# Kernel tuning notes

Hardware: AMD Instinct MI355X
Metric: run time of the kernel (lower is better)

The kernel has to match this reference:

```python
import jax, jax.numpy as jnp
import numpy as np

LN_EPS = 1e-5
SLOPE = 0.01  # LeakyReLU default

def _ln(x, g, b):
    m = x.mean(-1, keepdims=True)
    v = ((x - m) ** 2).mean(-1, keepdims=True)
    return (x - m) / jnp.sqrt(v + LN_EPS) * g + b

def _leaky(x):
    return jnp.where(x >= 0, x, SLOPE * x)

def _lstm(x_seq, h0, c0, Wih, Whh, bih, bhh):
    # x_seq: [B,S,E]; PyTorch gate order i,f,g,o. Returns (hT, per-step hiddens [B,S,H]).
    gx = jnp.einsum('bse,ge->bsg', x_seq, Wih) + bih + bhh  # precompute input projections
    def step(carry, gxt):
        h, c = carry
        gates = gxt + h @ Whh.T
        i, f, g, o = jnp.split(gates, 4, axis=-1)
        c = jax.nn.sigmoid(f) * c + jax.nn.sigmoid(i) * jnp.tanh(g)
        h = jax.nn.sigmoid(o) * jnp.tanh(c)
        return (h, c), h
    (hT, _), hs = jax.lax.scan(step, (h0, c0), gx.transpose(1, 0, 2))
    return hT, hs.transpose(1, 0, 2)

def setup_inputs() -> dict:
    B, S, NF, E, H, L, C = 256, 1024, 32, 64, 128, 64, 31
    key = jax.random.key(0)
    ks = iter(jax.random.split(key, 40))
    rn = lambda shape, s=0.08: (jax.random.normal(next(ks), shape, jnp.float32) * s)
    d = {}
    d['x'] = jax.random.normal(next(ks), (B, S, NF), jnp.float32)
    d['eps'] = jax.random.normal(next(ks), (B, L), jnp.float32)
    d['init_W'] = rn((E, NF)); d['init_b'] = rn((E,)); d['init_g'] = jnp.ones((E,)); d['init_beta'] = jnp.zeros((E,))
    d['enc_Wih'] = rn((4 * H, E)); d['enc_Whh'] = rn((4 * H, H)); d['enc_bih'] = rn((4 * H,)); d['enc_bhh'] = rn((4 * H,))
    d['mu_W'] = rn((L, H)); d['mu_b'] = rn((L,)); d['mu_g'] = jnp.ones((L,)); d['mu_beta'] = jnp.zeros((L,))
    d['lv_W'] = rn((L, H)); d['lv_b'] = rn((L,)); d['lv_g'] = jnp.ones((L,)); d['lv_beta'] = jnp.zeros((L,))
    d['dec_Wih'] = rn((4 * H, E)); d['dec_Whh'] = rn((4 * H, H)); d['dec_bih'] = rn((4 * H,)); d['dec_bhh'] = rn((4 * H,))
    d['lh_W'] = rn((H, L)); d['lh_b'] = rn((H,)); d['lh_g'] = jnp.ones((H,)); d['lh_beta'] = jnp.zeros((H,))
    d['lc_W'] = rn((H, L)); d['lc_b'] = rn((H,)); d['lc_g'] = jnp.ones((H,)); d['lc_beta'] = jnp.zeros((H,))
    d['act_W'] = rn((C, H)); d['act_b'] = rn((C,))
    d['time_W'] = rn((1, H)); d['time_b'] = rn((1,))
    return d

def reference(x, eps, init_W, init_b, init_g, init_beta,
              enc_Wih, enc_Whh, enc_bih, enc_bhh,
              mu_W, mu_b, mu_g, mu_beta, lv_W, lv_b, lv_g, lv_beta,
              dec_Wih, dec_Whh, dec_bih, dec_bhh,
              lh_W, lh_b, lh_g, lh_beta, lc_W, lc_b, lc_g, lc_beta,
              act_W, act_b, time_W, time_b):
    B = x.shape[0]
    H = enc_Whh.shape[1]
    # init_layers: Linear -> LeakyReLU -> LayerNorm
    x_emb = _ln(_leaky(x @ init_W.T + init_b), init_g, init_beta)  # [B,S,E]
    # encoder LSTM with h0=ones, c0=zeros (as in encode())
    hT, _ = _lstm(x_emb, jnp.ones((B, H), x.dtype), jnp.zeros((B, H), x.dtype),
                  enc_Wih, enc_Whh, enc_bih, enc_bhh)
    mu = _ln(_leaky(hT @ mu_W.T + mu_b), mu_g, mu_beta)
    logvar = _ln(_leaky(hT @ lv_W.T + lv_b), lv_g, lv_beta)
    latent = mu + eps * jnp.exp(0.5 * logvar)
    # decoder init state from latent
    dh0 = _ln(_leaky(latent @ lh_W.T + lh_b), lh_g, lh_beta)
    dc0 = _ln(_leaky(latent @ lc_W.T + lc_b), lc_g, lc_beta)
    # _decode prefix loop (prefix_len=1..S-1, collecting hn) == one scan over x_emb[:, :S-1]
    _, hs = _lstm(x_emb[:, :-1], dh0, dc0, dec_Wih, dec_Whh, dec_bih, dec_bhh)  # [B,S-1,H]
    acts = hs @ act_W.T + act_b   # [B,S-1,C]
    ts = hs @ time_W.T + time_b   # [B,S-1,1]
    return acts, ts, mu, logvar
```

## Files before the change

kernel.cpp:

```cpp
#include <hip/hip_runtime.h>
#include <hip/hip_bf16.h>
#include <type_traits>


#define B_ 256
#define S_ 1024
#define NF_ 32
#define E_ 64
#define H_ 128
#define L_ 64
#define C_ 31

#define ACTS_OFF 0
#define TS_OFF   8118528
#define MU_OFF   8380416
#define LV_OFF   8396800

#define LOG2E  1.44269504f
#define LOG2E2 2.88539008f

typedef __attribute__((ext_vector_type(8))) short short8;
typedef __attribute__((ext_vector_type(4))) float float4v;

__device__ inline unsigned short f2bf(float x){
  union { float f; unsigned u; } a; a.f = x;
  unsigned r = a.u + 0x7FFFu + ((a.u >> 16) & 1u);
  return (unsigned short)(r >> 16);
}
__device__ inline float frcp(float x){
#if __has_builtin(__builtin_amdgcn_rcpf)
  return __builtin_amdgcn_rcpf(x);
#else
  return 1.0f / x;
#endif
}
__device__ inline float fexp2(float x){
#if __has_builtin(__builtin_amdgcn_exp2f)
  return __builtin_amdgcn_exp2f(x);
#else
  return exp2f(x);
#endif
}
__device__ inline float fsig(float x){ return frcp(1.0f + fexp2(-LOG2E*x)); }
__device__ inline float leaky(float x){ return x >= 0.0f ? x : 0.01f*x; }
__device__ inline float wredsum(float v){
  v += __shfl_xor(v, 32, 64);
  v += __shfl_xor(v, 16, 64);
  v += __shfl_xor(v,  8, 64);
  v += __shfl_xor(v,  4, 64);
  v += __shfl_xor(v,  2, 64);
  v += __shfl_xor(v,  1, 64);
  return v;
}

#define INIT_ROWS 16
__global__ __launch_bounds__(256) void init_kernel(
    const float* __restrict__ x, const float* __restrict__ W,
    const float* __restrict__ bias, const float* __restrict__ gam,
    const float* __restrict__ beta, unsigned short* __restrict__ xemb)
{
  if (blockIdx.x == 0 && threadIdx.x < 64)
    xemb[(size_t)S_*B_*E_ + threadIdx.x] = 0;

  const int wave = threadIdx.x >> 6, lane = threadIdx.x & 63;
  float wf[NF_];
  {
    const float4* wr = (const float4*)(W + lane * NF_);
    #pragma unroll
    for (int j = 0; j < NF_/4; ++j){
      float4 t = wr[j];
      wf[4*j+0] = t.x; wf[4*j+1] = t.y; wf[4*j+2] = t.z; wf[4*j+3] = t.w;
    }
  }
  const float bb = bias[lane], gg = gam[lane], be = beta[lane];

  const int r0 = (blockIdx.x * 4 + wave) * INIT_ROWS;
  for (int rr = 0; rr < INIT_ROWS; ++rr){
    const int ru = __builtin_amdgcn_readfirstlane(r0 + rr);
    const int b = ru >> 10, s = ru & 1023;
    const float* xr = x + (size_t)ru * NF_;
    float acc = bb;
    #pragma unroll
    for (int k = 0; k < NF_; ++k)
      acc = fmaf(xr[k], wf[k], acc);
    acc = leaky(acc);
    float m = wredsum(acc) * (1.0f/64.0f);
    float d = acc - m;
    float v = wredsum(d*d) * (1.0f/64.0f);
    float y = d * rsqrtf(v + 1e-5f) * gg + be;
    xemb[((size_t)s * B_ + b) * E_ + lane] = f2bf(y);
  }
}

__global__ __launch_bounds__(512, 2) void lstm_kernel(
    const float* __restrict__ Wih,
    const float* __restrict__ Whh,
    const float* __restrict__ bih, const float* __restrict__ bhh,
    const unsigned short* __restrict__ xemb,
    int T,
    const float* __restrict__ h0, const float* __restrict__ c0,
    float* __restrict__ hT_out,
    float* __restrict__ outp,
    const float* __restrict__ actW, const float* __restrict__ actB,
    const float* __restrict__ timeW, const float* __restrict__ timeB)
{
  __shared__ unsigned short hbuf[2][16*136];
  const int tid = threadIdx.x;
  const int wave = tid >> 6, lane = tid & 63;
  const int q = lane >> 4, c16 = lane & 15;
  const int bt0 = blockIdx.x * 4;
  const int hu = wave * 16 + c16;

  short8 Bf[4][6];
  float bias[4];
  #pragma unroll
  for (int g = 0; g < 4; ++g){
    const int gcol = g*128 + hu;
    bias[g] = bih[gcol] + bhh[gcol];
    #pragma unroll
    for (int kb = 0; kb < 6; ++kb){
      union { short8 v; unsigned short u[8]; } tmp;
      #pragma unroll
      for (int j = 0; j < 8; ++j){
        int k = kb*32 + q*8 + j;
        float wv = (kb < 4) ? Whh[gcol*H_ + k] : Wih[gcol*E_ + (k - H_)];
        tmp.u[j] = f2bf(wv);
      }
      Bf[g][kb] = tmp.v;
    }
  }

  const bool do_out = (outp != nullptr) && (wave < 2);
  short8 Of0 = 0, Of1 = 0, Of2 = 0, Of3 = 0;
  float obias = 0.0f;
  if (do_out){
    const int n = wave*16 + c16;
    obias = (n < C_) ? actB[n] : timeB[0];
    union { short8 v; unsigned short u[8]; } tmp[4];
    #pragma unroll
    for (int kb = 0; kb < 4; ++kb)
      #pragma unroll
      for (int j = 0; j < 8; ++j){
        int k = kb*32 + q*8 + j;
        tmp[kb].u[j] = f2bf((n < C_) ? actW[n*H_ + k] : timeW[k]);
      }
    Of0 = tmp[0].v; Of1 = tmp[1].v; Of2 = tmp[2].v; Of3 = tmp[3].v;
  }

  unsigned short* hflat = &hbuf[0][0];
  for (int idx = tid; idx < 2*16*136; idx += 512) hflat[idx] = 0;
  __syncthreads();
  {
    int b = tid >> 7, k = tid & 127;
    hbuf[0][(4*b)*136 + k] = h0 ? f2bf(h0[((size_t)(bt0 + b))*H_ + k])
                                : (unsigned short)0x3F80;
  }
  float cst = c0 ? c0[((size_t)(bt0 + q))*H_ + hu] : 0.0f;
  __syncthreads();

  const int xb = c16 >> 2, xdt = c16 & 3;
  const unsigned short* xbase = xemb + ((size_t)(bt0 + xb))*E_ + q*8;
  const size_t xrow = (size_t)B_*E_;
  auto xwin = [&](int wt)->const unsigned short*{
    int tt = wt + xdt; if (tt > T-1) tt = T-1;
    return xbase + (size_t)tt * xrow;
  };

  float4v gxA[4], gxB[4];
  short8 nx0, nx1;
  { const unsigned short* p = xwin(0);
    nx0 = *(const short8*)p; nx1 = *(const short8*)(p + 32); }
  #pragma unroll
  for (int g = 0; g < 4; ++g){
    float4v t = (float4v){bias[g], bias[g], bias[g], bias[g]};
    t = __builtin_amdgcn_mfma_f32_16x16x32_bf16(nx0, Bf[g][4], t, 0, 0, 0);
    gxA[g] = __builtin_amdgcn_mfma_f32_16x16x32_bf16(nx1, Bf[g][5], t, 0, 0, 0);
  }
  { const unsigned short* p = xwin(4);
    nx0 = *(const short8*)p; nx1 = *(const short8*)(p + 32); }

  short8 Af0 = 0, Af1 = 0, Af2 = 0, Af3 = 0;
  short8 Po0 = 0, Po1 = 0, Po2 = 0, Po3 = 0;

  const unsigned short* haR0 = hflat + (c16 & ~3)*136 + q*8;
  const unsigned short* haR1 = haR0 + 2176;
  unsigned short* hw0 = hflat + (4*q)*136 + hu;
  unsigned short* hw1 = hw0 + 2176;
  float zero_f = 0.0f;
  const float4v z4 = (float4v){0.0f, 0.0f, 0.0f, 0.0f};

  auto out_head = [&](const unsigned short* ha, int tt_){
    if ((c16 & 3) == 0){
      Po0 = *(const short8*)(ha);
      Po1 = *(const short8*)(ha + 32);
      Po2 = *(const short8*)(ha + 64);
      Po3 = *(const short8*)(ha + 96);
    }
    float4v o = z4;
    o = __builtin_amdgcn_mfma_f32_16x16x32_bf16(Po0, Of0, o, 0, 0, 0);
    o = __builtin_amdgcn_mfma_f32_16x16x32_bf16(Po1, Of1, o, 0, 0, 0);
    o = __builtin_amdgcn_mfma_f32_16x16x32_bf16(Po2, Of2, o, 0, 0, 0);
    o = __builtin_amdgcn_mfma_f32_16x16x32_bf16(Po3, Of3, o, 0, 0, 0);
    const float val = o[0] + obias;
    const int n = wave*16 + c16;
    const size_t bq = (size_t)(bt0 + q);
    if (n < C_) outp[ACTS_OFF + (bq*(S_-1) + (size_t)tt_)*C_ + n] = val;
    else        outp[TS_OFF + bq*(S_-1) + (size_t)tt_] = val;
  };

  auto step = [&](int t, auto dtc, float4v (&gxP)[4], auto&& pre, auto&& post){
    constexpr int dt = decltype(dtc)::value;
    const unsigned short* ha = (t & 1) ? haR1 : haR0;
    if ((c16 & 3) == dt){
      Af0 = *(const short8*)(ha);
      Af1 = *(const short8*)(ha + 32);
      Af2 = *(const short8*)(ha + 64);
      Af3 = *(const short8*)(ha + 96);
    }
    pre();
    if (do_out && t > 0) out_head(ha, t - 1);

    float4v aA[4], aB[4];
    #pragma unroll
    for (int g = 0; g < 4; ++g)
      aA[g] = __builtin_amdgcn_mfma_f32_16x16x32_bf16(Af0, Bf[g][0], gxP[g], 0, 0, 0);
    #pragma unroll
    for (int g = 0; g < 4; ++g)
      aB[g] = __builtin_amdgcn_mfma_f32_16x16x32_bf16(Af2, Bf[g][2], z4, 0, 0, 0);
    #pragma unroll
    for (int g = 0; g < 4; ++g)
      aA[g] = __builtin_amdgcn_mfma_f32_16x16x32_bf16(Af1, Bf[g][1], aA[g], 0, 0, 0);
    #pragma unroll
    for (int g = 0; g < 4; ++g)
      aB[g] = __builtin_amdgcn_mfma_f32_16x16x32_bf16(Af3, Bf[g][3], aB[g], 0, 0, 0);

    post();

    float gi = aA[0][dt] + aB[0][dt];
    float gf = aA[1][dt] + aB[1][dt];
    float gg = aA[2][dt] + aB[2][dt];
    float go = aA[3][dt] + aB[3][dt];
    float ei  = fexp2(gi * LOG2E);
    float e2g = fexp2(gg * LOG2E2);
    float t1  = (ei * (e2g - 1.0f)) * frcp((1.0f + ei) * (1.0f + e2g));
    float sf  = fsig(gf);
    float c   = fmaf(sf, cst, t1);
    cst = c;
    float eo  = fexp2(go * LOG2E);
    float e2c = fexp2(fminf(c * LOG2E2, 126.0f));
    float h   = (eo * (e2c - 1.0f)) * frcp((1.0f + eo) * (1.0f + e2c));
    unsigned vv;
    asm("v_cvt_pk_bf16_f32 %0, %1, %2" : "=v"(vv) : "v"(h), "v"(zero_f));
    unsigned short hb16 = (unsigned short)vv;
    unsigned short* hw = (t & 1) ? hw0 : hw1;
    hw[0] = hb16;
    if (hT_out && t == T-1) hT_out[((size_t)(bt0 + q))*H_ + hu] = h;
    __builtin_amdgcn_sched_barrier(0);
    asm volatile("s_waitcnt lgkmcnt(0)" ::: "memory");
    __builtin_amdgcn_s_barrier();
    __builtin_amdgcn_sched_barrier(0);
  };

  using I0 = std::integral_constant<int,0>;
  using I1 = std::integral_constant<int,1>;
  using I2 = std::integral_constant<int,2>;
  using I3 = std::integral_constant<int,3>;
  auto nop = []{};

  const int nwin = T >> 2, ntail = T & 3;
  for (int w = 0; w < nwin; ++w){
    const int t0 = w << 2;
    step(t0+0, I0{}, gxA, [&]{
      #pragma unroll
      for (int g = 0; g < 4; ++g){
        float4v tt = (float4v){bias[g], bias[g], bias[g], bias[g]};
        tt = __builtin_amdgcn_mfma_f32_16x16x32_bf16(nx0, Bf[g][4], tt, 0, 0, 0);
        gxB[g] = __builtin_amdgcn_mfma_f32_16x16x32_bf16(nx1, Bf[g][5], tt, 0, 0, 0);
      }
    }, nop);
    step(t0+1, I1{}, gxA, [&]{
      const unsigned short* p = xwin(t0 + 8);
      nx0 = *(const short8*)p; nx1 = *(const short8*)(p + 32);
    }, nop);
    step(t0+2, I2{}, gxA, nop, nop);
    step(t0+3, I3{}, gxA, nop, [&]{
      #pragma unroll
      for (int g = 0; g < 4; ++g) gxA[g] = gxB[g];
    });
  }
  if (ntail > 0) step(nwin*4+0, I0{}, gxA, nop, nop);
  if (ntail > 1) step(nwin*4+1, I1{}, gxA, nop, nop);
  if (ntail > 2) step(nwin*4+2, I2{}, gxA, nop, nop);

  if (do_out) out_head((T & 1) ? haR1 : haR0, T - 1);
}

__global__ __launch_bounds__(128) void latent_kernel(
    const float* __restrict__ hT, const float* __restrict__ eps,
    const float* __restrict__ mu_W, const float* __restrict__ mu_b,
    const float* __restrict__ mu_g, const float* __restrict__ mu_be,
    const float* __restrict__ lv_W, const float* __restrict__ lv_b,
    const float* __restrict__ lv_g, const float* __restrict__ lv_be,
    const float* __restrict__ lh_W, const float* __restrict__ lh_b,
    const float* __restrict__ lh_g, const float* __restrict__ lh_be,
    const float* __restrict__ lc_W, const float* __restrict__ lc_b,
    const float* __restrict__ lc_g, const float* __restrict__ lc_be,
    float* __restrict__ out, float* __restrict__ dh0, float* __restrict__ dc0)
{
  const int b = blockIdx.x, tid = threadIdx.x;
  const int wave = tid >> 6, lane = tid & 63;
  __shared__ float shT[H_];
  __shared__ float smu[L_], slv[L_], slat[L_];
  __shared__ float part[2];
  shT[tid] = hT[(size_t)b*H_ + tid];
  __syncthreads();
  {
    const float* W = wave ? lv_W : mu_W;
    float a = (wave ? lv_b : mu_b)[lane];
    for (int k = 0; k < H_; ++k) a += shT[k] * W[lane*H_ + k];
    a = leaky(a);
    float m = wredsum(a) * (1.0f/L_);
    float d = a - m;
    float v = wredsum(d*d) * (1.0f/L_);
    float y = d * rsqrtf(v + 1e-5f) * (wave ? lv_g : mu_g)[lane] + (wave ? lv_be : mu_be)[lane];
    out[(wave ? LV_OFF : MU_OFF) + (size_t)b*L_ + lane] = y;
    if (wave) slv[lane] = y; else smu[lane] = y;
  }
  __syncthreads();
  if (tid < L_) slat[tid] = smu[tid] + eps[(size_t)b*L_ + tid] * expf(0.5f*slv[tid]);
  __syncthreads();
  #pragma unroll 1
  for (int which = 0; which < 2; ++which){
    const float* W = which ? lc_W : lh_W;
    float p = (which ? lc_b : lh_b)[tid];
    for (int k = 0; k < L_; ++k) p += slat[k] * W[tid*L_ + k];
    p = leaky(p);
    float s = wredsum(p);
    if (lane == 0) part[wave] = s;
    __syncthreads();
    float mean = (part[0] + part[1]) * (1.0f/H_);
    __syncthreads();
    float d = p - mean;
    float s2 = wredsum(d*d);
    if (lane == 0) part[wave] = s2;
    __syncthreads();
    float var = (part[0] + part[1]) * (1.0f/H_);
    __syncthreads();
    float y = d * rsqrtf(var + 1e-5f) * (which ? lc_g : lh_g)[tid] + (which ? lc_be : lh_be)[tid];
    (which ? dc0 : dh0)[(size_t)b*H_ + tid] = y;
  }
}

extern "C" void kernel_launch(void* const* d_in, const int* in_sizes, int n_in,
                              void* d_out, int out_size, void* d_ws, size_t ws_size,
                              hipStream_t stream)
{
  (void)in_sizes; (void)n_in; (void)out_size; (void)ws_size;
  const float* x       = (const float*)d_in[0];
  const float* eps     = (const float*)d_in[1];
  const float* init_W  = (const float*)d_in[2];
  const float* init_b  = (const float*)d_in[3];
  const float* init_g  = (const float*)d_in[4];
  const float* init_be = (const float*)d_in[5];
  const float* enc_Wih = (const float*)d_in[6];
  const float* enc_Whh = (const float*)d_in[7];
  const float* enc_bih = (const float*)d_in[8];
  const float* enc_bhh = (const float*)d_in[9];
  const float* mu_W  = (const float*)d_in[10];
  const float* mu_b  = (const float*)d_in[11];
  const float* mu_g  = (const float*)d_in[12];
  const float* mu_be = (const float*)d_in[13];
  const float* lv_W  = (const float*)d_in[14];
  const float* lv_b  = (const float*)d_in[15];
  const float* lv_g  = (const float*)d_in[16];
  const float* lv_be = (const float*)d_in[17];
  const float* dec_Wih = (const float*)d_in[18];
  const float* dec_Whh = (const float*)d_in[19];
  const float* dec_bih = (const float*)d_in[20];
  const float* dec_bhh = (const float*)d_in[21];
  const float* lh_W  = (const float*)d_in[22];
  const float* lh_b  = (const float*)d_in[23];
  const float* lh_g  = (const float*)d_in[24];
  const float* lh_be = (const float*)d_in[25];
  const float* lc_W  = (const float*)d_in[26];
  const float* lc_b  = (const float*)d_in[27];
  const float* lc_g  = (const float*)d_in[28];
  const float* lc_be = (const float*)d_in[29];
  const float* act_W  = (const float*)d_in[30];
  const float* act_b  = (const float*)d_in[31];
  const float* time_W = (const float*)d_in[32];
  const float* time_b = (const float*)d_in[33];
  float* out = (float*)d_out;

  unsigned short* xemb = (unsigned short*)d_ws;
  float* hT  = (float*)(xemb + (size_t)S_*B_*E_ + 64);
  float* dh0 = hT  + B_*H_;
  float* dc0 = dh0 + B_*H_;

  init_kernel<<<dim3((B_*S_)/(4*INIT_ROWS)), dim3(256), 0, stream>>>(
      x, init_W, init_b, init_g, init_be, xemb);

  lstm_kernel<<<dim3(64), dim3(512), 0, stream>>>(
      enc_Wih, enc_Whh, enc_bih, enc_bhh, xemb, S_,
      nullptr, nullptr, hT,
      nullptr, nullptr, nullptr, nullptr, nullptr);

  latent_kernel<<<dim3(B_), dim3(128), 0, stream>>>(
      hT, eps, mu_W, mu_b, mu_g, mu_be, lv_W, lv_b, lv_g, lv_be,
      lh_W, lh_b, lh_g, lh_be, lc_W, lc_b, lc_g, lc_be, out, dh0, dc0);

  lstm_kernel<<<dim3(64), dim3(512), 0, stream>>>(
      dec_Wih, dec_Whh, dec_bih, dec_bhh, xemb, S_-1,
      dh0, dc0, nullptr,
      out, act_W, act_b, time_W, time_b);
}
```

Baseline: 1.220 ms.

## Fuse encoder, latent, and decoder into one persistent kernel with batched output head

Merges the encoder LSTM, latent/LayerNorm stage, and decoder LSTM into a single kernel. Intermediate state (hT, dh0, dc0) stays in shared memory, which removes two launches and the global round-trips between them. The per-step output head is replaced by a history buffer in shared memory, so one MFMA sequence produces four timesteps of acts/ts every four steps instead of one output per step. This adds shared-memory use and register pressure, and the latent stage now runs on only 64 blocks.

```diff
diff --git a/kernel.cpp b/kernel.cpp
--- a/kernel.cpp
+++ b/kernel.cpp
@@ -92,211 +92,13 @@
   }
 }
 
-__global__ __launch_bounds__(512, 2) void lstm_kernel(
-    const float* __restrict__ Wih,
-    const float* __restrict__ Whh,
-    const float* __restrict__ bih, const float* __restrict__ bhh,
+__global__ __launch_bounds__(512, 2) void mega_kernel(
     const unsigned short* __restrict__ xemb,
-    int T,
-    const float* __restrict__ h0, const float* __restrict__ c0,
-    float* __restrict__ hT_out,
-    float* __restrict__ outp,
-    const float* __restrict__ actW, const float* __restrict__ actB,
-    const float* __restrict__ timeW, const float* __restrict__ timeB)
-{
-  __shared__ unsigned short hbuf[2][16*136];
-  const int tid = threadIdx.x;
-  const int wave = tid >> 6, lane = tid & 63;
-  const int q = lane >> 4, c16 = lane & 15;
-  const int bt0 = blockIdx.x * 4;
-  const int hu = wave * 16 + c16;
-
-  short8 Bf[4][6];
-  float bias[4];
-  #pragma unroll
-  for (int g = 0; g < 4; ++g){
-    const int gcol = g*128 + hu;
-    bias[g] = bih[gcol] + bhh[gcol];
-    #pragma unroll
-    for (int kb = 0; kb < 6; ++kb){
-      union { short8 v; unsigned short u[8]; } tmp;
-      #pragma unroll
-      for (int j = 0; j < 8; ++j){
-        int k = kb*32 + q*8 + j;
-        float wv = (kb < 4) ? Whh[gcol*H_ + k] : Wih[gcol*E_ + (k - H_)];
-        tmp.u[j] = f2bf(wv);
-      }
-      Bf[g][kb] = tmp.v;
-    }
-  }
-
-  const bool do_out = (outp != nullptr) && (wave < 2);
-  short8 Of0 = 0, Of1 = 0, Of2 = 0, Of3 = 0;
-  float obias = 0.0f;
-  if (do_out){
-    const int n = wave*16 + c16;
-    obias = (n < C_) ? actB[n] : timeB[0];
-    union { short8 v; unsigned short u[8]; } tmp[4];
-    #pragma unroll
-    for (int kb = 0; kb < 4; ++kb)
-      #pragma unroll
-      for (int j = 0; j < 8; ++j){
-        int k = kb*32 + q*8 + j;
-        tmp[kb].u[j] = f2bf((n < C_) ? actW[n*H_ + k] : timeW[k]);
-      }
-    Of0 = tmp[0].v; Of1 = tmp[1].v; Of2 = tmp[2].v; Of3 = tmp[3].v;
-  }
-
-  unsigned short* hflat = &hbuf[0][0];
-  for (int idx = tid; idx < 2*16*136; idx += 512) hflat[idx] = 0;
-  __syncthreads();
-  {
-    int b = tid >> 7, k = tid & 127;
-    hbuf[0][(4*b)*136 + k] = h0 ? f2bf(h0[((size_t)(bt0 + b))*H_ + k])
-                                : (unsigned short)0x3F80;
-  }
-  float cst = c0 ? c0[((size_t)(bt0 + q))*H_ + hu] : 0.0f;
-  __syncthreads();
-
-  const int xb = c16 >> 2, xdt = c16 & 3;
-  const unsigned short* xbase = xemb + ((size_t)(bt0 + xb))*E_ + q*8;
-  const size_t xrow = (size_t)B_*E_;
-  auto xwin = [&](int wt)->const unsigned short*{
-    int tt = wt + xdt; if (tt > T-1) tt = T-1;
-    return xbase + (size_t)tt * xrow;
-  };
-
-  float4v gxA[4], gxB[4];
-  short8 nx0, nx1;
-  { const unsigned short* p = xwin(0);
-    nx0 = *(const short8*)p; nx1 = *(const short8*)(p + 32); }
-  #pragma unroll
-  for (int g = 0; g < 4; ++g){
-    float4v t = (float4v){bias[g], bias[g], bias[g], bias[g]};
-    t = __builtin_amdgcn_mfma_f32_16x16x32_bf16(nx0, Bf[g][4], t, 0, 0, 0);
-    gxA[g] = __builtin_amdgcn_mfma_f32_16x16x32_bf16(nx1, Bf[g][5], t, 0, 0, 0);
-  }
-  { const unsigned short* p = xwin(4);
-    nx0 = *(const short8*)p; nx1 = *(const short8*)(p + 32); }
-
-  short8 Af0 = 0, Af1 = 0, Af2 = 0, Af3 = 0;
-  short8 Po0 = 0, Po1 = 0, Po2 = 0, Po3 = 0;
-
-  const unsigned short* haR0 = hflat + (c16 & ~3)*136 + q*8;
-  const unsigned short* haR1 = haR0 + 2176;
-  unsigned short* hw0 = hflat + (4*q)*136 + hu;
-  unsigned short* hw1 = hw0 + 2176;
-  float zero_f = 0.0f;
-  const float4v z4 = (float4v){0.0f, 0.0f, 0.0f, 0.0f};
-
-  auto out_head = [&](const unsigned short* ha, int tt_){
-    if ((c16 & 3) == 0){
-      Po0 = *(const short8*)(ha);
-      Po1 = *(const short8*)(ha + 32);
-      Po2 = *(const short8*)(ha + 64);
-      Po3 = *(const short8*)(ha + 96);
-    }
-    float4v o = z4;
-    o = __builtin_amdgcn_mfma_f32_16x16x32_bf16(Po0, Of0, o, 0, 0, 0);
-    o = __builtin_amdgcn_mfma_f32_16x16x32_bf16(Po1, Of1, o, 0, 0, 0);
-    o = __builtin_amdgcn_mfma_f32_16x16x32_bf16(Po2, Of2, o, 0, 0, 0);
-    o = __builtin_amdgcn_mfma_f32_16x16x32_bf16(Po3, Of3, o, 0, 0, 0);
-    const float val = o[0] + obias;
-    const int n = wave*16 + c16;
-    const size_t bq = (size_t)(bt0 + q);
-    if (n < C_) outp[ACTS_OFF + (bq*(S_-1) + (size_t)tt_)*C_ + n] = val;
-    else        outp[TS_OFF + bq*(S_-1) + (size_t)tt_] = val;
-  };
-
-  auto step = [&](int t, auto dtc, float4v (&gxP)[4], auto&& pre, auto&& post){
-    constexpr int dt = decltype(dtc)::value;
-    const unsigned short* ha = (t & 1) ? haR1 : haR0;
-    if ((c16 & 3) == dt){
-      Af0 = *(const short8*)(ha);
-      Af1 = *(const short8*)(ha + 32);
-      Af2 = *(const short8*)(ha + 64);
-      Af3 = *(const short8*)(ha + 96);
-    }
-    pre();
-    if (do_out && t > 0) out_head(ha, t - 1);
-
-    float4v aA[4], aB[4];
-    #pragma unroll
-    for (int g = 0; g < 4; ++g)
-      aA[g] = __builtin_amdgcn_mfma_f32_16x16x32_bf16(Af0, Bf[g][0], gxP[g], 0, 0, 0);
-    #pragma unroll
-    for (int g = 0; g < 4; ++g)
-      aB[g] = __builtin_amdgcn_mfma_f32_16x16x32_bf16(Af2, Bf[g][2], z4, 0, 0, 0);
-    #pragma unroll
-    for (int g = 0; g < 4; ++g)
-      aA[g] = __builtin_amdgcn_mfma_f32_16x16x32_bf16(Af1, Bf[g][1], aA[g], 0, 0, 0);
-    #pragma unroll
-    for (int g = 0; g < 4; ++g)
-      aB[g] = __builtin_amdgcn_mfma_f32_16x16x32_bf16(Af3, Bf[g][3], aB[g], 0, 0, 0);
-
-    post();
-
-    float gi = aA[0][dt] + aB[0][dt];
-    float gf = aA[1][dt] + aB[1][dt];
-    float gg = aA[2][dt] + aB[2][dt];
-    float go = aA[3][dt] + aB[3][dt];
-    float ei  = fexp2(gi * LOG2E);
-    float e2g = fexp2(gg * LOG2E2);
-    float t1  = (ei * (e2g - 1.0f)) * frcp((1.0f + ei) * (1.0f + e2g));
-    float sf  = fsig(gf);
-    float c   = fmaf(sf, cst, t1);
-    cst = c;
-    float eo  = fexp2(go * LOG2E);
-    float e2c = fexp2(fminf(c * LOG2E2, 126.0f));
-    float h   = (eo * (e2c - 1.0f)) * frcp((1.0f + eo) * (1.0f + e2c));
-    unsigned vv;
-    asm("v_cvt_pk_bf16_f32 %0, %1, %2" : "=v"(vv) : "v"(h), "v"(zero_f));
-    unsigned short hb16 = (unsigned short)vv;
-    unsigned short* hw = (t & 1) ? hw0 : hw1;
-    hw[0] = hb16;
-    if (hT_out && t == T-1) hT_out[((size_t)(bt0 + q))*H_ + hu] = h;
-    __builtin_amdgcn_sched_barrier(0);
-    asm volatile("s_waitcnt lgkmcnt(0)" ::: "memory");
-    __builtin_amdgcn_s_barrier();
-    __builtin_amdgcn_sched_barrier(0);
-  };
-
-  using I0 = std::integral_constant<int,0>;
-  using I1 = std::integral_constant<int,1>;
-  using I2 = std::integral_constant<int,2>;
-  using I3 = std::integral_constant<int,3>;
-  auto nop = []{};
-
-  const int nwin = T >> 2, ntail = T & 3;
-  for (int w = 0; w < nwin; ++w){
-    const int t0 = w << 2;
-    step(t0+0, I0{}, gxA, [&]{
-      #pragma unroll
-      for (int g = 0; g < 4; ++g){
-        float4v tt = (float4v){bias[g], bias[g], bias[g], bias[g]};
-        tt = __builtin_amdgcn_mfma_f32_16x16x32_bf16(nx0, Bf[g][4], tt, 0, 0, 0);
-        gxB[g] = __builtin_amdgcn_mfma_f32_16x16x32_bf16(nx1, Bf[g][5], tt, 0, 0, 0);
-      }
-    }, nop);
-    step(t0+1, I1{}, gxA, [&]{
-      const unsigned short* p = xwin(t0 + 8);
-      nx0 = *(const short8*)p; nx1 = *(const short8*)(p + 32);
-    }, nop);
-    step(t0+2, I2{}, gxA, nop, nop);
-    step(t0+3, I3{}, gxA, nop, [&]{
-      #pragma unroll
-      for (int g = 0; g < 4; ++g) gxA[g] = gxB[g];
-    });
-  }
-  if (ntail > 0) step(nwin*4+0, I0{}, gxA, nop, nop);
-  if (ntail > 1) step(nwin*4+1, I1{}, gxA, nop, nop);
-  if (ntail > 2) step(nwin*4+2, I2{}, gxA, nop, nop);
-
-  if (do_out) out_head((T & 1) ? haR1 : haR0, T - 1);
-}
-
-__global__ __launch_bounds__(128) void latent_kernel(
-    const float* __restrict__ hT, const float* __restrict__ eps,
+    const float* __restrict__ encWih, const float* __restrict__ encWhh,
+    const float* __restrict__ encbih, const float* __restrict__ encbhh,
+    const float* __restrict__ decWih, const float* __restrict__ decWhh,
+    const float* __restrict__ decbih, const float* __restrict__ decbhh,
+    const float* __restrict__ eps,
     const float* __restrict__ mu_W, const float* __restrict__ mu_b,
     const float* __restrict__ mu_g, const float* __restrict__ mu_be,
     const float* __restrict__ lv_W, const float* __restrict__ lv_b,
@@ -305,50 +107,293 @@
     const float* __restrict__ lh_g, const float* __restrict__ lh_be,
     const float* __restrict__ lc_W, const float* __restrict__ lc_b,
     const float* __restrict__ lc_g, const float* __restrict__ lc_be,
-    float* __restrict__ out, float* __restrict__ dh0, float* __restrict__ dc0)
+    const float* __restrict__ actW, const float* __restrict__ actB,
+    const float* __restrict__ timeW, const float* __restrict__ timeB,
+    float* __restrict__ out)
 {
-  const int b = blockIdx.x, tid = threadIdx.x;
+  __shared__ unsigned short hbuf[2][16*136];
+  __shared__ unsigned short hist[2][16*136];
+  __shared__ float shT[4][H_];
+  __shared__ float sml[4][2*L_];
+  __shared__ float slat[4][L_];
+  __shared__ float sdh[4][H_], sdc[4][H_];
+  __shared__ float partA[8];
+
+  const int tid = threadIdx.x;
   const int wave = tid >> 6, lane = tid & 63;
-  __shared__ float shT[H_];
-  __shared__ float smu[L_], slv[L_], slat[L_];
-  __shared__ float part[2];
-  shT[tid] = hT[(size_t)b*H_ + tid];
+  const int q = lane >> 4, c16 = lane & 15;
+  const int bt0 = blockIdx.x * 4;
+  const int hu = wave * 16 + c16;
+  unsigned short* hflat = &hbuf[0][0];
+  unsigned short* histf = &hist[0][0];
+  const float4v z4 = (float4v){0.0f, 0.0f, 0.0f, 0.0f};
+  float zero_f = 0.0f;
+
+  for (int idx = tid; idx < 2*16*136; idx += 512) hflat[idx] = 0;
   __syncthreads();
+
+  const int xb = c16 >> 2, xdt = c16 & 3;
+  const unsigned short* xbase = xemb + ((size_t)(bt0 + xb))*E_ + q*8;
+  const size_t xrow = (size_t)B_*E_;
+
+  using I0 = std::integral_constant<int,0>;
+  using I1 = std::integral_constant<int,1>;
+  using I2 = std::integral_constant<int,2>;
+  using I3 = std::integral_constant<int,3>;
+  auto nop = []{};
+
+  auto run = [&](const float* Wih, const float* Whh, const float* bih,
+                 const float* bhh, int T, auto decc){
+    constexpr bool DEC = decltype(decc)::value;
+
+    short8 Bf[4][6];
+    float bias[4];
+    #pragma unroll
+    for (int g = 0; g < 4; ++g){
+      const int gcol = g*128 + hu;
+      bias[g] = bih[gcol] + bhh[gcol];
+      #pragma unroll
+      for (int kb = 0; kb < 6; ++kb){
+        union { short8 v; unsigned short u[8]; } tmp;
+        #pragma unroll
+        for (int j = 0; j < 8; ++j){
+          int k = kb*32 + q*8 + j;
+          float wv = (kb < 4) ? Whh[gcol*H_ + k] : Wih[gcol*E_ + (k - H_)];
+          tmp.u[j] = f2bf(wv);
+        }
+        Bf[g][kb] = tmp.v;
+      }
+    }
+
+    const bool do_head = DEC && (wave < 2);
+    short8 Of0 = 0, Of1 = 0, Of2 = 0, Of3 = 0;
+    float obias = 0.0f;
+    if (do_head){
+      const int n = wave*16 + c16;
+      obias = (n < C_) ? actB[n] : timeB[0];
+      union { short8 v; unsigned short u[8]; } tmp[4];
+      #pragma unroll
+      for (int kb = 0; kb < 4; ++kb)
+        #pragma unroll
+        for (int j = 0; j < 8; ++j){
+          int k = kb*32 + q*8 + j;
+          tmp[kb].u[j] = f2bf((n < C_) ? actW[n*H_ + k] : timeW[k]);
+        }
+      Of0 = tmp[0].v; Of1 = tmp[1].v; Of2 = tmp[2].v; Of3 = tmp[3].v;
+    }
+    short8 Ph0 = 0, Ph1 = 0, Ph2 = 0, Ph3 = 0;
+    float4v oacc = z4;
+
+    {
+      int b = tid >> 7, k = tid & 127;
+      hbuf[0][(4*b)*136 + k] = DEC ? f2bf(sdh[b][k]) : (unsigned short)0x3F80;
+    }
+    float cst = DEC ? sdc[q][hu] : 0.0f;
+    __syncthreads();
+
+    auto xwin = [&](int wt)->const unsigned short*{
+      int tt = wt + xdt; if (tt > T-1) tt = T-1;
+      return xbase + (size_t)tt * xrow;
+    };
+
+    float4v gxA[4], gxB[4];
+    short8 nx0, nx1;
+    { const unsigned short* p = xwin(0);
+      nx0 = *(const short8*)p; nx1 = *(const short8*)(p + 32); }
+    #pragma unroll
+    for (int g = 0; g < 4; ++g){
+      float4v t = (float4v){bias[g], bias[g], bias[g], bias[g]};
+      t = __builtin_amdgcn_mfma_f32_16x16x32_bf16(nx0, Bf[g][4], t, 0, 0, 0);
+      gxA[g] = __builtin_amdgcn_mfma_f32_16x16x32_bf16(nx1, Bf[g][5], t, 0, 0, 0);
+    }
+    { const unsigned short* p = xwin(4);
+      nx0 = *(const short8*)p; nx1 = *(const short8*)(p + 32); }
+
+    short8 Af0 = 0, Af1 = 0, Af2 = 0, Af3 = 0;
+
+    const unsigned short* haR0 = hflat + (c16 & ~3)*136 + q*8;
+    const unsigned short* haR1 = haR0 + 2176;
+    unsigned short* hw0 = hflat + (4*q)*136 + hu;
+    unsigned short* hw1 = hw0 + 2176;
+
+    auto step = [&](int t, auto dtc, float4v (&gxP)[4], auto&& pre, auto&& post){
+      constexpr int dt = decltype(dtc)::value;
+      const unsigned short* ha = (t & 1) ? haR1 : haR0;
+      if ((c16 & 3) == dt){
+        Af0 = *(const short8*)(ha);
+        Af1 = *(const short8*)(ha + 32);
+        Af2 = *(const short8*)(ha + 64);
+        Af3 = *(const short8*)(ha + 96);
+      }
+      pre();
+
+      float4v aA[4], aB[4];
+      #pragma unroll
+      for (int g = 0; g < 4; ++g)
+        aA[g] = __builtin_amdgcn_mfma_f32_16x16x32_bf16(Af0, Bf[g][0], gxP[g], 0, 0, 0);
+      #pragma unroll
+      for (int g = 0; g < 4; ++g)
+        aB[g] = __builtin_amdgcn_mfma_f32_16x16x32_bf16(Af2, Bf[g][2], z4, 0, 0, 0);
+      #pragma unroll
+      for (int g = 0; g < 4; ++g)
+        aA[g] = __builtin_amdgcn_mfma_f32_16x16x32_bf16(Af1, Bf[g][1], aA[g], 0, 0, 0);
+      #pragma unroll
+      for (int g = 0; g < 4; ++g)
+        aB[g] = __builtin_amdgcn_mfma_f32_16x16x32_bf16(Af3, Bf[g][3], aB[g], 0, 0, 0);
+
+      post();
+
+      float gi = aA[0][dt] + aB[0][dt];
+      float gf = aA[1][dt] + aB[1][dt];
+      float gg = aA[2][dt] + aB[2][dt];
+      float go = aA[3][dt] + aB[3][dt];
+      float ei  = fexp2(gi * LOG2E);
+      float e2g = fexp2(gg * LOG2E2);
+      float t1  = (ei * (e2g - 1.0f)) * frcp((1.0f + ei) * (1.0f + e2g));
+      float sf  = fsig(gf);
+      float c   = fmaf(sf, cst, t1);
+      cst = c;
+      float eo  = fexp2(go * LOG2E);
+      float e2c = fexp2(fminf(c * LOG2E2, 126.0f));
+      float h   = (eo * (e2c - 1.0f)) * frcp((1.0f + eo) * (1.0f + e2c));
+      unsigned vv;
+      asm("v_cvt_pk_bf16_f32 %0, %1, %2" : "=v"(vv) : "v"(h), "v"(zero_f));
+      unsigned short hb16 = (unsigned short)vv;
+      unsigned short* hw = (t & 1) ? hw0 : hw1;
+      hw[0] = hb16;
+      if (DEC)
+        histf[((t >> 2) & 1)*2176 + (4*q + dt)*136 + hu] = hb16;
+      if (!DEC && t == T-1) shT[q][hu] = h;
+      __builtin_amdgcn_sched_barrier(0);
+      asm volatile("s_waitcnt lgkmcnt(0)" ::: "memory");
+      __builtin_amdgcn_s_barrier();
+      __builtin_amdgcn_sched_barrier(0);
+    };
+
+    auto head_mfma = [&](int par){
+      const unsigned short* hb = histf + par*2176 + c16*136 + q*8;
+      Ph0 = *(const short8*)(hb);
+      Ph1 = *(const short8*)(hb + 32);
+      Ph2 = *(const short8*)(hb + 64);
+      Ph3 = *(const short8*)(hb + 96);
+      float4v o = (float4v){obias, obias, obias, obias};
+      o = __builtin_amdgcn_mfma_f32_16x16x32_bf16(Ph0, Of0, o, 0, 0, 0);
+      o = __builtin_amdgcn_mfma_f32_16x16x32_bf16(Ph1, Of1, o, 0, 0, 0);
+      o = __builtin_amdgcn_mfma_f32_16x16x32_bf16(Ph2, Of2, o, 0, 0, 0);
+      o = __builtin_amdgcn_mfma_f32_16x16x32_bf16(Ph3, Of3, o, 0, 0, 0);
+      oacc = o;
+    };
+    auto head_store = [&](int tb, int cnt){
+      const int n = wave*16 + c16;
+      const size_t bq = (size_t)(bt0 + q);
+      if (n < C_){
+        #pragma unroll
+        for (int r = 0; r < 4; ++r)
+          if (r < cnt) out[ACTS_OFF + (bq*(size_t)(S_-1) + (size_t)(tb + r))*C_ + n] = oacc[r];
+      } else {
+        #pragma unroll
+        for (int r = 0; r < 4; ++r)
+          if (r < cnt) out[TS_OFF + bq*(size_t)(S_-1) + (size_t)(tb + r)] = oacc[r];
+      }
+    };
+
+    const int nwin = T >> 2, ntail = T & 3;
+    for (int w = 0; w < nwin; ++w){
+      const int t0 = w << 2;
+      step(t0+0, I0{}, gxA, [&]{
+        #pragma unroll
+        for (int g = 0; g < 4; ++g){
+          float4v tt = (float4v){bias[g], bias[g], bias[g], bias[g]};
+          tt = __builtin_amdgcn_mfma_f32_16x16x32_bf16(nx0, Bf[g][4], tt, 0, 0, 0);
+          gxB[g] = __builtin_amdgcn_mfma_f32_16x16x32_bf16(nx1, Bf[g][5], tt, 0, 0, 0);
+        }
+      }, nop);
+      step(t0+1, I1{}, gxA, [&]{
+        const unsigned short* p = xwin(t0 + 8);
+        nx0 = *(const short8*)p; nx1 = *(const short8*)(p + 32);
+      }, nop);
+      step(t0+2, I2{}, gxA, [&]{
+        if (do_head && w > 0) head_mfma((w-1) & 1);
+      }, nop);
+      step(t0+3, I3{}, gxA, [&]{
+        if (do_head && w > 0) head_store((w-1)*4, 4);
+      }, [&]{
+        #pragma unroll
+        for (int g = 0; g < 4; ++g) gxA[g] = gxB[g];
+      });
+    }
+    if (ntail > 0) step(nwin*4+0, I0{}, gxA, [&]{
+        if (do_head) head_mfma((nwin-1) & 1);
+      }, nop);
+    if (ntail > 1) step(nwin*4+1, I1{}, gxA, [&]{
+        if (do_head) head_store((nwin-1)*4, 4);
+      }, nop);
+    if (ntail > 2) step(nwin*4+2, I2{}, gxA, nop, nop);
+    if (do_head && ntail > 0){
+      head_mfma(nwin & 1);
+      head_store(nwin*4, ntail);
+    }
+  };
+
+  run(encWih, encWhh, encbih, encbhh, S_, std::integral_constant<bool,false>{});
+
   {
-    const float* W = wave ? lv_W : mu_W;
-    float a = (wave ? lv_b : mu_b)[lane];
-    for (int k = 0; k < H_; ++k) a += shT[k] * W[lane*H_ + k];
+    const int bb = tid >> 7, slot = tid & 127;
+    const int unit = slot & 63;
+    const bool isLv = slot >= 64;
+    const float* W = isLv ? lv_W : mu_W;
+    float a = (isLv ? lv_b : mu_b)[unit];
+    const float4* wr = (const float4*)(W + unit*H_);
+    #pragma unroll 4
+    for (int j = 0; j < H_/4; ++j){
+      float4 w4 = wr[j];
+      a += w4.x*shT[bb][4*j] + w4.y*shT[bb][4*j+1]
+         + w4.z*shT[bb][4*j+2] + w4.w*shT[bb][4*j+3];
+    }
     a = leaky(a);
     float m = wredsum(a) * (1.0f/L_);
     float d = a - m;
     float v = wredsum(d*d) * (1.0f/L_);
-    float y = d * rsqrtf(v + 1e-5f) * (wave ? lv_g : mu_g)[lane] + (wave ? lv_be : mu_be)[lane];
-    out[(wave ? LV_OFF : MU_OFF) + (size_t)b*L_ + lane] = y;
-    if (wave) slv[lane] = y; else smu[lane] = y;
+    float y = d * rsqrtf(v + 1e-5f) * (isLv ? lv_g : mu_g)[unit]
+            + (isLv ? lv_be : mu_be)[unit];
+    out[(isLv ? LV_OFF : MU_OFF) + (size_t)(bt0 + bb)*L_ + unit] = y;
+    sml[bb][slot] = y;
+    __syncthreads();
+    if (!isLv)
+      slat[bb][unit] = sml[bb][unit]
+                     + eps[(size_t)(bt0 + bb)*L_ + unit] * expf(0.5f*sml[bb][64 + unit]);
+    __syncthreads();
+    #pragma unroll 1
+    for (int which = 0; which < 2; ++which){
+      const float* W2 = which ? lc_W : lh_W;
+      float p = (which ? lc_b : lh_b)[slot];
+      const float4* w2 = (const float4*)(W2 + slot*L_);
+      #pragma unroll 4
+      for (int j = 0; j < L_/4; ++j){
+        float4 w4 = w2[j];
+        p += w4.x*slat[bb][4*j] + w4.y*slat[bb][4*j+1]
+           + w4.z*slat[bb][4*j+2] + w4.w*slat[bb][4*j+3];
+      }
+      p = leaky(p);
+      float s = wredsum(p);
+      if (lane == 0) partA[wave] = s;
+      __syncthreads();
+      float mean = (partA[2*bb] + partA[2*bb+1]) * (1.0f/H_);
+      __syncthreads();
+      float dd = p - mean;
+      float s2 = wredsum(dd*dd);
+      if (lane == 0) partA[wave] = s2;
+      __syncthreads();
+      float var = (partA[2*bb] + partA[2*bb+1]) * (1.0f/H_);
+      __syncthreads();
+      float yy = dd * rsqrtf(var + 1e-5f) * (which ? lc_g : lh_g)[slot]
+               + (which ? lc_be : lh_be)[slot];
+      (which ? sdc : sdh)[bb][slot] = yy;
+    }
   }
   __syncthreads();
-  if (tid < L_) slat[tid] = smu[tid] + eps[(size_t)b*L_ + tid] * expf(0.5f*slv[tid]);
-  __syncthreads();
-  #pragma unroll 1
-  for (int which = 0; which < 2; ++which){
-    const float* W = which ? lc_W : lh_W;
-    float p = (which ? lc_b : lh_b)[tid];
-    for (int k = 0; k < L_; ++k) p += slat[k] * W[tid*L_ + k];
-    p = leaky(p);
-    float s = wredsum(p);
-    if (lane == 0) part[wave] = s;
-    __syncthreads();
-    float mean = (part[0] + part[1]) * (1.0f/H_);
-    __syncthreads();
-    float d = p - mean;
-    float s2 = wredsum(d*d);
-    if (lane == 0) part[wave] = s2;
-    __syncthreads();
-    float var = (part[0] + part[1]) * (1.0f/H_);
-    __syncthreads();
-    float y = d * rsqrtf(var + 1e-5f) * (which ? lc_g : lh_g)[tid] + (which ? lc_be : lh_be)[tid];
-    (which ? dc0 : dh0)[(size_t)b*H_ + tid] = y;
-  }
+
+  run(decWih, decWhh, decbih, decbhh, S_-1, std::integral_constant<bool,true>{});
 }
 
 extern "C" void kernel_launch(void* const* d_in, const int* in_sizes, int n_in,
@@ -393,24 +438,19 @@
   float* out = (float*)d_out;
 
   unsigned short* xemb = (unsigned short*)d_ws;
-  float* hT  = (float*)(xemb + (size_t)S_*B_*E_ + 64);
-  float* dh0 = hT  + B_*H_;
-  float* dc0 = dh0 + B_*H_;
 
   init_kernel<<<dim3((B_*S_)/(4*INIT_ROWS)), dim3(256), 0, stream>>>(
       x, init_W, init_b, init_g, init_be, xemb);
 
-  lstm_kernel<<<dim3(64), dim3(512), 0, stream>>>(
-      enc_Wih, enc_Whh, enc_bih, enc_bhh, xemb, S_,
-      nullptr, nullptr, hT,
-      nullptr, nullptr, nullptr, nullptr, nullptr);
-
-  latent_kernel<<<dim3(B_), dim3(128), 0, stream>>>(
-      hT, eps, mu_W, mu_b, mu_g, mu_be, lv_W, lv_b, lv_g, lv_be,
-      lh_W, lh_b, lh_g, lh_be, lc_W, lc_b, lc_g, lc_be, out, dh0, dc0);
-
-  lstm_kernel<<<dim3(64), dim3(512), 0, stream>>>(
-      dec_Wih, dec_Whh, dec_bih, dec_bhh, xemb, S_-1,
-      dh0, dc0, nullptr,
-      out, act_W, act_b, time_W, time_b);
-}
+  mega_kernel<<<dim3(64), dim3(512), 0, stream>>>(
+      xemb,
+      enc_Wih, enc_Whh, enc_bih, enc_bhh,
+      dec_Wih, dec_Whh, dec_bih, dec_bhh,
+      eps,
+      mu_W, mu_b, mu_g, mu_be,
+      lv_W, lv_b, lv_g, lv_be,
+      lh_W, lh_b, lh_g, lh_be,
+      lc_W, lc_b, lc_g, lc_be,
+      act_W, act_b, time_W, time_b,
+      out);
+}
```

After: 1.203 ms. No clear change (-1.4%).
